# Optimization experiments

Hardware: AMD Instinct MI355X
Metric: run time of the kernel (lower is better)

## Reference

```python
import jax, jax.numpy as jnp
import numpy as np

B, S, HID = 1, 2048, 2048
H, HKV, D = 32, 8, 64
G = H // HKV  # query heads per kv head


def rotate_half(x):
    x1, x2 = jnp.split(x, 2, axis=-1)
    return jnp.concatenate([-x2, x1], axis=-1)


def setup_inputs() -> dict:
    key = jax.random.key(0)
    ks = jax.random.split(key, 7)
    hidden_states = jax.random.normal(ks[0], (B, S, HID), dtype=jnp.float32)
    # RoPE tables (any broadcastable values work for correctness; use real angles)
    inv_freq = 1.0 / (10000.0 ** (np.arange(0, D, 2, dtype=np.float32) / D))
    ang = np.arange(S, dtype=np.float32)[:, None] * inv_freq[None, :]  # [S, D/2]
    ang = np.concatenate([ang, ang], axis=-1)  # [S, D]
    cos = jnp.asarray(np.cos(ang))[None, None]  # [1,1,S,D]
    sin = jnp.asarray(np.sin(ang))[None, None]
    sc = 0.02
    Wq = jax.random.normal(ks[1], (H * D, HID), dtype=jnp.float32) * sc
    Wk = jax.random.normal(ks[2], (HKV * D, HID), dtype=jnp.float32) * sc
    Wv = jax.random.normal(ks[3], (HKV * D, HID), dtype=jnp.float32) * sc
    Wo = jax.random.normal(ks[4], (HID, H * D), dtype=jnp.float32) * sc
    return {"hidden_states": hidden_states, "cos": cos, "sin": sin,
            "Wq": Wq, "Wk": Wk, "Wv": Wv, "Wo": Wo}


def reference(hidden_states, cos, sin, Wq, Wk, Wv, Wo):
    b, s, _ = hidden_states.shape
    # projections (torch Linear: x @ W^T)
    q = jnp.einsum('bsh,oh->bso', hidden_states, Wq).reshape(b, s, H, D).transpose(0, 2, 1, 3)   # [B,H,S,D]
    k = jnp.einsum('bsh,oh->bso', hidden_states, Wk).reshape(b, s, HKV, D).transpose(0, 2, 1, 3)  # [B,Hkv,S,D]
    v = jnp.einsum('bsh,oh->bso', hidden_states, Wv).reshape(b, s, HKV, D).transpose(0, 2, 1, 3)
    # RoPE
    q = q * cos + rotate_half(q) * sin
    k = k * cos + rotate_half(k) * sin
    # GQA: group query heads instead of repeat_interleave-ing KV
    qg = q.reshape(b, HKV, G, s, D)
    scores = jnp.einsum('bkgsd,bktd->bkgst', qg, k) / jnp.sqrt(jnp.asarray(D, q.dtype))
    causal = jnp.tril(jnp.ones((s, s), dtype=bool))
    scores = jnp.where(causal, scores, jnp.asarray(-jnp.inf, scores.dtype))
    probs = jax.nn.softmax(scores.astype(jnp.float32), axis=-1).astype(q.dtype)
    ctx = jnp.einsum('bkgst,bktd->bkgsd', probs, v)  # [B,Hkv,G,S,D]
    ctx = ctx.reshape(b, H, s, D).transpose(0, 2, 1, 3).reshape(b, s, H * D)
    return jnp.einsum('bso,ho->bsh', ctx, Wo)
```

## Files before the change

kernel.cpp:

```cpp
#include <hip/hip_runtime.h>

typedef unsigned short u16;
typedef __bf16 bf16x8 __attribute__((ext_vector_type(8)));
typedef float f32x4 __attribute__((ext_vector_type(4)));
typedef float f32x16 __attribute__((ext_vector_type(16)));

static __device__ __forceinline__ u16 f2bf(float f) {
  unsigned u = __builtin_bit_cast(unsigned, f);
  u += 0x7fffu + ((u >> 16) & 1u);
  return (u16)(u >> 16);
}
static __device__ __forceinline__ float bf2f(u16 u) {
  return __builtin_bit_cast(float, (unsigned)u << 16);
}
static __device__ __forceinline__ unsigned cvtpk(float lo, float hi) {
  unsigned r;
  asm("v_cvt_pk_bf16_f32 %0, %1, %2" : "=v"(r) : "v"(lo), "v"(hi));
  return r;
}
static __device__ __forceinline__ float fexp2(float x) {
  float r;
  asm("v_exp_f32 %0, %1" : "=v"(r) : "v"(x));
  return r;
}

static __device__ __forceinline__ void gload_lds16(const void* g, void* l) {
  __builtin_amdgcn_global_load_lds((const __attribute__((address_space(1))) unsigned int*)g,
                                   (__attribute__((address_space(3))) unsigned int*)l,
                                   16, 0, 0);
}

__global__ __launch_bounds__(256) void cvt_all(
    const float* __restrict__ X, const float* __restrict__ Wq, const float* __restrict__ Wk,
    const float* __restrict__ Wv, const float* __restrict__ Wo,
    u16* __restrict__ oX, u16* __restrict__ oWq, u16* __restrict__ oWk,
    u16* __restrict__ oWv, u16* __restrict__ oWo) {
  const int b = blockIdx.x;
  const float* s; u16* d; int lb;
  if (b < 1024)      { s = X;  d = oX;  lb = b; }
  else if (b < 2048) { s = Wq; d = oWq; lb = b - 1024; }
  else if (b < 2304) { s = Wk; d = oWk; lb = b - 2048; }
  else if (b < 2560) { s = Wv; d = oWv; lb = b - 2304; }
  else               { s = Wo; d = oWo; lb = b - 2560; }
  const int base = lb * 4096 + threadIdx.x * 4;
#pragma unroll
  for (int j = 0; j < 4; ++j) {
    const int off = base + j * 1024;
    float4 v = *(const float4*)(s + off);
    ushort4 u;
    u.x = f2bf(v.x); u.y = f2bf(v.y); u.z = f2bf(v.z); u.w = f2bf(v.w);
    *(ushort4*)(d + off) = u;
  }
}

__global__ __launch_bounds__(256, 4) void gemm_qkv(
    const u16* __restrict__ A, const u16* __restrict__ Bq, const u16* __restrict__ Bk,
    const u16* __restrict__ Bv, u16* __restrict__ Qb, u16* __restrict__ Kb,
    u16* __restrict__ Vt, const float* __restrict__ cosp, const float* __restrict__ sinp) {
  __shared__ u16 As[64 * 64];
  __shared__ u16 Bs[128 * 64];
  const int tid = threadIdx.x;
  const int lane = tid & 63, w = tid >> 6;
  const int wr = w >> 1, wc = w & 1;
  const int lr = lane & 15, lq = lane >> 4;
  const int bm = blockIdx.y << 6;
  const int bn = blockIdx.x << 7;
  const int K = 2048;

  const u16* Bp; int nb, region;
  if (bn < 2048)      { Bp = Bq; nb = bn;        region = 0; }
  else if (bn < 2560) { Bp = Bk; nb = bn - 2048; region = 1; }
  else                { Bp = Bv; nb = bn - 2560; region = 2; }

  f32x4 acc[2][4] = {};

  for (int kt = 0; kt < 32; ++kt) {
    const int k0 = kt << 6;
#pragma unroll
    for (int i = 0; i < 2; ++i) {
      const int cid = (i << 8) + tid;
      const int r = cid >> 3, c = cid & 7;
      const int cs = (c ^ (r & 7)) << 3;
      gload_lds16(A + (size_t)(bm + r) * K + k0 + cs, (char*)As + cid * 16);
    }
#pragma unroll
    for (int i = 0; i < 4; ++i) {
      const int cid = (i << 8) + tid;
      const int r = cid >> 3, c = cid & 7;
      const int cs = (c ^ (r & 7)) << 3;
      gload_lds16(Bp + (size_t)(nb + r) * K + k0 + cs, (char*)Bs + cid * 16);
    }
    __syncthreads();
    bf16x8 af[2][2], bfv[2][4];
#pragma unroll
    for (int ks = 0; ks < 2; ++ks) {
#pragma unroll
      for (int f = 0; f < 2; ++f) {
        const int ra = wr * 32 + f * 16 + lr;
        const int ca = (lq + (ks << 2)) ^ (ra & 7);
        af[ks][f] = *(const bf16x8*)&As[((ra << 3) | ca) << 3];
      }
#pragma unroll
      for (int f = 0; f < 4; ++f) {
        const int rb = wc * 64 + f * 16 + lr;
        const int cb = (lq + (ks << 2)) ^ (rb & 7);
        bfv[ks][f] = *(const bf16x8*)&Bs[((rb << 3) | cb) << 3];
      }
    }
#pragma unroll
    for (int ks = 0; ks < 2; ++ks)
#pragma unroll
      for (int mf = 0; mf < 2; ++mf)
#pragma unroll
        for (int nf = 0; nf < 4; ++nf)
          acc[mf][nf] = __builtin_amdgcn_mfma_f32_16x16x32_bf16(
              af[ks][mf], bfv[ks][nf], acc[mf][nf], 0, 0, 0);
    __syncthreads();
  }

  const int rbase = bm + wr * 32;
  const int cb64 = nb + wc * 64;
  if (region == 2) {
    const int hkv = cb64 >> 6;
#pragma unroll
    for (int mf = 0; mf < 2; ++mf) {
      const int s0 = rbase + mf * 16 + lq * 4;
#pragma unroll
      for (int nf = 0; nf < 4; ++nf) {
        const int d = (cb64 & 63) + nf * 16 + lr;
        ushort4 st;
        st.x = f2bf(acc[mf][nf][0]); st.y = f2bf(acc[mf][nf][1]);
        st.z = f2bf(acc[mf][nf][2]); st.w = f2bf(acc[mf][nf][3]);
        *(ushort4*)&Vt[(size_t)hkv * 131072 + (size_t)d * 2048 + s0] = st;
      }
    }
  } else {
    u16* outp = region ? Kb : Qb;
    const int ldo = region ? 512 : 2048;
    const float post = region ? 1.0f : 0.18033688011112042f;
#pragma unroll
    for (int mf = 0; mf < 2; ++mf)
#pragma unroll
      for (int r = 0; r < 4; ++r) {
        const int s = rbase + mf * 16 + lq * 4 + r;
        const float* cr = cosp + s * 64;
        const float* sr = sinp + s * 64;
#pragma unroll
        for (int nf = 0; nf < 2; ++nf) {
          const int d1 = nf * 16 + lr, d2 = d1 + 32;
          const float x1 = acc[mf][nf][r], x2 = acc[mf][nf + 2][r];
          const float y1 = (x1 * cr[d1] - x2 * sr[d1]) * post;
          const float y2 = (x2 * cr[d2] + x1 * sr[d2]) * post;
          outp[(size_t)s * ldo + cb64 + d1] = f2bf(y1);
          outp[(size_t)s * ldo + cb64 + d2] = f2bf(y2);
        }
      }
  }
}

__global__ __launch_bounds__(256, 4) void gemm_out(
    const u16* __restrict__ A, const u16* __restrict__ B, float* __restrict__ C,
    int M, int N, int K) {
  __shared__ u16 As[64 * 64];
  __shared__ u16 Bs[128 * 64];
  const int tid = threadIdx.x;
  const int lane = tid & 63, w = tid >> 6;
  const int wr = w >> 1, wc = w & 1;
  const int lr = lane & 15, lq = lane >> 4;
  const int bm = blockIdx.y << 6, bn = blockIdx.x << 7;

  f32x4 acc[2][4] = {};
  const int nK = K >> 6;
  for (int kt = 0; kt < nK; ++kt) {
    const int k0 = kt << 6;
#pragma unroll
    for (int i = 0; i < 2; ++i) {
      const int cid = (i << 8) + tid;
      const int r = cid >> 3, c = cid & 7;
      const int cs = (c ^ (r & 7)) << 3;
      gload_lds16(A + (size_t)(bm + r) * K + k0 + cs, (char*)As + cid * 16);
    }
#pragma unroll
    for (int i = 0; i < 4; ++i) {
      const int cid = (i << 8) + tid;
      const int r = cid >> 3, c = cid & 7;
      const int cs = (c ^ (r & 7)) << 3;
      gload_lds16(B + (size_t)(bn + r) * K + k0 + cs, (char*)Bs + cid * 16);
    }
    __syncthreads();
    bf16x8 af[2][2], bfv[2][4];
#pragma unroll
    for (int ks = 0; ks < 2; ++ks) {
#pragma unroll
      for (int f = 0; f < 2; ++f) {
        const int ra = wr * 32 + f * 16 + lr;
        const int ca = (lq + (ks << 2)) ^ (ra & 7);
        af[ks][f] = *(const bf16x8*)&As[((ra << 3) | ca) << 3];
      }
#pragma unroll
      for (int f = 0; f < 4; ++f) {
        const int rb = wc * 64 + f * 16 + lr;
        const int cb = (lq + (ks << 2)) ^ (rb & 7);
        bfv[ks][f] = *(const bf16x8*)&Bs[((rb << 3) | cb) << 3];
      }
    }
#pragma unroll
    for (int ks = 0; ks < 2; ++ks)
#pragma unroll
      for (int mf = 0; mf < 2; ++mf)
#pragma unroll
        for (int nf = 0; nf < 4; ++nf)
          acc[mf][nf] = __builtin_amdgcn_mfma_f32_16x16x32_bf16(
              af[ks][mf], bfv[ks][nf], acc[mf][nf], 0, 0, 0);
    __syncthreads();
  }
  const int rbase = bm + wr * 32;
  const int cbase = bn + wc * 64;
#pragma unroll
  for (int mf = 0; mf < 2; ++mf)
#pragma unroll
    for (int r = 0; r < 4; ++r) {
      const int s = rbase + mf * 16 + lq * 4 + r;
#pragma unroll
      for (int nf = 0; nf < 4; ++nf)
        C[(size_t)s * N + cbase + nf * 16 + lr] = acc[mf][nf][r];
    }
}

__global__ __launch_bounds__(256, 4) void attn_v11(
    const u16* __restrict__ Qb, const u16* __restrict__ Kb,
    const u16* __restrict__ Vt, u16* __restrict__ P0, u16* __restrict__ P1,
    u16* __restrict__ P2, float* __restrict__ lsum) {
  __shared__ u16 Ks[2][4096];
  __shared__ u16 Vs[2][4096];
  const int qb = 63 - (int)blockIdx.x;
  const int hkv = blockIdx.y;
  const int ck = blockIdx.z;
  const int tid = threadIdx.x;
  const int w = tid >> 6, lane = tid & 63;
  const int col = lane & 31, hi = lane >> 5;
  const int g = col >> 3, r = col & 7;
  const int h = hkv * 4 + g;

  const int nt = (qb >> 1) + 1;
  const int q0w = qb * 32 + w * 8;
  const int qg = q0w + r;

  u16* Pc = (ck == 0) ? P0 : (ck == 1) ? P1 : P2;

  const u16* qp = Qb + (size_t)qg * 2048 + h * 64 + hi * 8;
  uint4 qf[4];
#pragma unroll
  for (int s = 0; s < 4; ++s) qf[s] = *(const uint4*)(qp + 16 * s);

  f32x16 o0 = {}, o1 = {};
  float l_loc = 0.f;

  auto STAGE = [&](int buf, int t) {
    const int kv0 = t << 6;
#pragma unroll
    for (int i = 0; i < 2; ++i) {
      const int cid = i * 256 + tid;
      const int rr = cid >> 3, cc = cid & 7;
      const int csw = (cc ^ (rr & 7)) << 3;
      gload_lds16(Kb + (size_t)(kv0 + rr) * 512 + hkv * 64 + csw,
                  (char*)Ks + buf * 8192 + cid * 16);
      gload_lds16(Vt + (size_t)hkv * 131072 + (size_t)rr * 2048 + kv0 + csw,
                  (char*)Vs + buf * 8192 + cid * 16);
    }
  };

  if (ck < nt) {
    STAGE(0, ck);
    int i = 0;
    for (int t = ck; t < nt; t += 3, ++i) {
      const int buf = i & 1;
      __syncthreads();
      if (t + 3 < nt) STAGE(buf ^ 1, t + 3);
      const char* Kl = (const char*)Ks + buf * 8192;
      const char* Vl = (const char*)Vs + buf * 8192;

      f32x16 sc0 = {}, sc1 = {};
#pragma unroll
      for (int s = 0; s < 4; ++s) {
        const int c = 2 * s + hi;
        const bf16x8 k0 = *(const bf16x8*)(Kl + (((col) << 3) + (c ^ (col & 7))) * 16);
        sc0 = __builtin_amdgcn_mfma_f32_32x32x16_bf16(
            k0, __builtin_bit_cast(bf16x8, qf[s]), sc0, 0, 0, 0);
        const bf16x8 k1 = *(const bf16x8*)(Kl + (((col + 32) << 3) + (c ^ (col & 7))) * 16);
        sc1 = __builtin_amdgcn_mfma_f32_32x32x16_bf16(
            k1, __builtin_bit_cast(bf16x8, qf[s]), sc1, 0, 0, 0);
      }

      if (t == nt - 1) {
        const int qoff = ((qb & 1) << 5) + w * 8 + r;
#pragma unroll
        for (int i2 = 0; i2 < 16; ++i2) {
          const int kvr = (i2 & 3) + 8 * (i2 >> 2) + 4 * hi;
          if (kvr > qoff) sc0[i2] = -1e30f;
          if (kvr + 32 > qoff) sc1[i2] = -1e30f;
        }
      }

      float p0[16], p1[16];
#pragma unroll
      for (int i2 = 0; i2 < 16; ++i2) { p0[i2] = fexp2(sc0[i2]); p1[i2] = fexp2(sc1[i2]); }

      float r0 = 0.f, r1 = 0.f, r2 = 0.f, r3 = 0.f;
#pragma unroll
      for (int i2 = 0; i2 < 4; ++i2) {
        r0 += p0[4 * i2]     + p1[4 * i2];
        r1 += p0[4 * i2 + 1] + p1[4 * i2 + 1];
        r2 += p0[4 * i2 + 2] + p1[4 * i2 + 2];
        r3 += p0[4 * i2 + 3] + p1[4 * i2 + 3];
      }
      l_loc += (r0 + r1) + (r2 + r3);

      unsigned W0a[4], W1a[4], W0b[4], W1b[4];
#pragma unroll
      for (int gg = 0; gg < 4; ++gg) {
        W0a[gg] = cvtpk(p0[4 * gg], p0[4 * gg + 1]);
        W1a[gg] = cvtpk(p0[4 * gg + 2], p0[4 * gg + 3]);
        W0b[gg] = cvtpk(p1[4 * gg], p1[4 * gg + 1]);
        W1b[gg] = cvtpk(p1[4 * gg + 2], p1[4 * gg + 3]);
      }

#pragma unroll
      for (int s2 = 0; s2 < 4; ++s2) {
        const unsigned* W0 = (s2 & 2) ? W0b : W0a;
        const unsigned* W1 = (s2 & 2) ? W1b : W1a;
        const int G = s2 & 1, ga = 2 * G, gb = 2 * G + 1;
        const unsigned sx0 = hi ? W0[ga] : W0[gb];
        const unsigned sx1 = hi ? W1[ga] : W1[gb];
        const unsigned rx0 = __shfl_xor(sx0, 32, 64);
        const unsigned rx1 = __shfl_xor(sx1, 32, 64);
        uint4 pw;
        pw.x = hi ? rx0 : W0[ga];
        pw.y = hi ? rx1 : W1[ga];
        pw.z = hi ? W0[gb] : rx0;
        pw.w = hi ? W1[gb] : rx1;
        const bf16x8 pf = __builtin_bit_cast(bf16x8, pw);
        const int c = 2 * s2 + hi;
        const bf16x8 v0 = *(const bf16x8*)(Vl + (((col) << 3) + (c ^ (col & 7))) * 16);
        const bf16x8 v1 = *(const bf16x8*)(Vl + (((col + 32) << 3) + (c ^ (col & 7))) * 16);
        o0 = __builtin_amdgcn_mfma_f32_32x32x16_bf16(v0, pf, o0, 0, 0, 0);
        o1 = __builtin_amdgcn_mfma_f32_32x32x16_bf16(v1, pf, o1, 0, 0, 0);
      }
    }
  }

  const float l = l_loc + __shfl_xor(l_loc, 32, 64);

  u16* op = Pc + (size_t)qg * 2048 + h * 64;
#pragma unroll
  for (int gg = 0; gg < 4; ++gg) {
    uint2 s0, s1;
    s0.x = cvtpk(o0[4 * gg], o0[4 * gg + 1]);
    s0.y = cvtpk(o0[4 * gg + 2], o0[4 * gg + 3]);
    s1.x = cvtpk(o1[4 * gg], o1[4 * gg + 1]);
    s1.y = cvtpk(o1[4 * gg + 2], o1[4 * gg + 3]);
    *(uint2*)(op + 8 * gg + 4 * hi)      = s0;
    *(uint2*)(op + 8 * gg + 4 * hi + 32) = s1;
  }
  if (hi == 0)
    lsum[(size_t)ck * 65536 + (size_t)qg * 32 + h] = l;
}

__global__ __launch_bounds__(256) void attn_merge3(
    u16* __restrict__ P0, const u16* __restrict__ P1, const u16* __restrict__ P2,
    const float* __restrict__ lsum) {
  const int s = blockIdx.x;
  const int e0 = threadIdx.x * 8;
  const int h = e0 >> 6;
  const float l = lsum[(size_t)s * 32 + h] + lsum[65536 + (size_t)s * 32 + h] +
                  lsum[131072 + (size_t)s * 32 + h];
  const float inv = 1.f / l;
  uint4 a = *(const uint4*)(P0 + (size_t)s * 2048 + e0);
  uint4 b = *(const uint4*)(P1 + (size_t)s * 2048 + e0);
  uint4 d = *(const uint4*)(P2 + (size_t)s * 2048 + e0);
  const u16* pa = (const u16*)&a;
  const u16* pb = (const u16*)&b;
  const u16* pd = (const u16*)&d;
  ushort4 oA, oB;
  oA.x = f2bf((bf2f(pa[0]) + bf2f(pb[0]) + bf2f(pd[0])) * inv);
  oA.y = f2bf((bf2f(pa[1]) + bf2f(pb[1]) + bf2f(pd[1])) * inv);
  oA.z = f2bf((bf2f(pa[2]) + bf2f(pb[2]) + bf2f(pd[2])) * inv);
  oA.w = f2bf((bf2f(pa[3]) + bf2f(pb[3]) + bf2f(pd[3])) * inv);
  oB.x = f2bf((bf2f(pa[4]) + bf2f(pb[4]) + bf2f(pd[4])) * inv);
  oB.y = f2bf((bf2f(pa[5]) + bf2f(pb[5]) + bf2f(pd[5])) * inv);
  oB.z = f2bf((bf2f(pa[6]) + bf2f(pb[6]) + bf2f(pd[6])) * inv);
  oB.w = f2bf((bf2f(pa[7]) + bf2f(pb[7]) + bf2f(pd[7])) * inv);
  *(ushort4*)(P0 + (size_t)s * 2048 + e0)     = oA;
  *(ushort4*)(P0 + (size_t)s * 2048 + e0 + 4) = oB;
}

extern "C" void kernel_launch(void* const* d_in, const int* in_sizes, int n_in,
                              void* d_out, int out_size, void* d_ws, size_t ws_size,
                              hipStream_t stream) {
  const float* X    = (const float*)d_in[0];
  const float* cosp = (const float*)d_in[1];
  const float* sinp = (const float*)d_in[2];
  const float* Wq   = (const float*)d_in[3];
  const float* Wk   = (const float*)d_in[4];
  const float* Wv   = (const float*)d_in[5];
  const float* Wo   = (const float*)d_in[6];

  u16* ws  = (u16*)d_ws;
  u16* Xb  = ws;
  u16* Wqb = ws + 4194304;
  u16* Wkb = ws + 8388608;
  u16* Wvb = ws + 9437184;
  u16* Wob = ws + 10485760;
  u16* Qb  = ws + 14680064;
  u16* Kb  = ws + 18874368;
  u16* Vt  = ws + 19922944;
  u16* P2  = ws + 20971520;
  u16* P0  = Xb;
  u16* P1  = Wqb;
  float* lsum = (float*)(ws + 8388608);

  cvt_all<<<3584, 256, 0, stream>>>(X, Wq, Wk, Wv, Wo, Xb, Wqb, Wkb, Wvb, Wob);

  dim3 gqkv(24, 32), ga(64, 8, 3), go(16, 32);
  gemm_qkv<<<gqkv, 256, 0, stream>>>(Xb, Wqb, Wkb, Wvb, Qb, Kb, Vt, cosp, sinp);
  attn_v11<<<ga, 256, 0, stream>>>(Qb, Kb, Vt, P0, P1, P2, lsum);
  attn_merge3<<<2048, 256, 0, stream>>>(P0, P1, P2, lsum);
  gemm_out<<<go, 16 * 16, 0, stream>>>(P0, Wob, (float*)d_out, 2048, 2048, 2048);
}
```

Before: 128.5 us.

## Use 512-thread attention blocks covering 64 query rows with balanced block ordering

Result: faster. 122.2 us (-4.9%).

```diff
diff --git a/kernel.cpp b/kernel.cpp
--- a/kernel.cpp
+++ b/kernel.cpp
@@ -227,24 +227,24 @@
     }
 }
 
-__global__ __launch_bounds__(256, 4) void attn_v11(
+__global__ __launch_bounds__(512, 4) void attn_v12(
     const u16* __restrict__ Qb, const u16* __restrict__ Kb,
     const u16* __restrict__ Vt, u16* __restrict__ P0, u16* __restrict__ P1,
     u16* __restrict__ P2, float* __restrict__ lsum) {
   __shared__ u16 Ks[2][4096];
   __shared__ u16 Vs[2][4096];
-  const int qb = 63 - (int)blockIdx.x;
-  const int hkv = blockIdx.y;
-  const int ck = blockIdx.z;
+  const int hkv = blockIdx.x / 3;
+  const int ck = blockIdx.x % 3;
+  const int by = blockIdx.y;
+  const int j = (by & 1) ? (by >> 1) : (31 - (by >> 1));
   const int tid = threadIdx.x;
   const int w = tid >> 6, lane = tid & 63;
   const int col = lane & 31, hi = lane >> 5;
   const int g = col >> 3, r = col & 7;
   const int h = hkv * 4 + g;
 
-  const int nt = (qb >> 1) + 1;
-  const int q0w = qb * 32 + w * 8;
-  const int qg = q0w + r;
+  const int qoff = w * 8 + r;
+  const int qg = j * 64 + qoff;
 
   u16* Pc = (ck == 0) ? P0 : (ck == 1) ? P1 : P2;
 
@@ -258,25 +258,21 @@
 
   auto STAGE = [&](int buf, int t) {
     const int kv0 = t << 6;
-#pragma unroll
-    for (int i = 0; i < 2; ++i) {
-      const int cid = i * 256 + tid;
-      const int rr = cid >> 3, cc = cid & 7;
-      const int csw = (cc ^ (rr & 7)) << 3;
-      gload_lds16(Kb + (size_t)(kv0 + rr) * 512 + hkv * 64 + csw,
-                  (char*)Ks + buf * 8192 + cid * 16);
-      gload_lds16(Vt + (size_t)hkv * 131072 + (size_t)rr * 2048 + kv0 + csw,
-                  (char*)Vs + buf * 8192 + cid * 16);
-    }
+    const int rr = tid >> 3, cc = tid & 7;
+    const int csw = (cc ^ (rr & 7)) << 3;
+    gload_lds16(Kb + (size_t)(kv0 + rr) * 512 + hkv * 64 + csw,
+                (char*)Ks + buf * 8192 + tid * 16);
+    gload_lds16(Vt + (size_t)hkv * 131072 + (size_t)rr * 2048 + kv0 + csw,
+                (char*)Vs + buf * 8192 + tid * 16);
   };
 
-  if (ck < nt) {
+  if (ck <= j) {
     STAGE(0, ck);
     int i = 0;
-    for (int t = ck; t < nt; t += 3, ++i) {
+    for (int t = ck; t <= j; t += 3, ++i) {
       const int buf = i & 1;
       __syncthreads();
-      if (t + 3 < nt) STAGE(buf ^ 1, t + 3);
+      if (t + 3 <= j) STAGE(buf ^ 1, t + 3);
       const char* Kl = (const char*)Ks + buf * 8192;
       const char* Vl = (const char*)Vs + buf * 8192;
 
@@ -292,8 +288,7 @@
             k1, __builtin_bit_cast(bf16x8, qf[s]), sc1, 0, 0, 0);
       }
 
-      if (t == nt - 1) {
-        const int qoff = ((qb & 1) << 5) + w * 8 + r;
+      if (t == j) {
 #pragma unroll
         for (int i2 = 0; i2 < 16; ++i2) {
           const int kvr = (i2 & 3) + 8 * (i2 >> 2) + 4 * hi;
@@ -421,9 +416,9 @@
 
   cvt_all<<<3584, 256, 0, stream>>>(X, Wq, Wk, Wv, Wo, Xb, Wqb, Wkb, Wvb, Wob);
 
-  dim3 gqkv(24, 32), ga(64, 8, 3), go(16, 32);
+  dim3 gqkv(24, 32), ga(24, 32), go(16, 32);
   gemm_qkv<<<gqkv, 256, 0, stream>>>(Xb, Wqb, Wkb, Wvb, Qb, Kb, Vt, cosp, sinp);
-  attn_v11<<<ga, 256, 0, stream>>>(Qb, Kb, Vt, P0, P1, P2, lsum);
+  attn_v12<<<ga, 512, 0, stream>>>(Qb, Kb, Vt, P0, P1, P2, lsum);
   attn_merge3<<<2048, 256, 0, stream>>>(P0, P1, P2, lsum);
-  gemm_out<<<go, 16 * 16, 0, stream>>>(P0, Wob, (float*)d_out, 2048, 2048, 2048);
-}
+  gemm_out<<<go, 256, 0, stream>>>(P0, Wob, (float*)d_out, 2048, 2048, 2048);
+}
```
